# Kernel optimization log

Hardware: AMD Instinct MI355X
Metric: run time of the kernel (lower is better)

The kernel has to match this reference:

```python
import jax, jax.numpy as jnp
import numpy as np

# Sampled-block sizes (fanouts [25, 10], batch of 1024 seeds)
N_SRC1, N_DST1, N_E1 = 292864, 11264, 281600
N_DST2, N_E2 = 1024, 10240
IN, H, C = 256, 256, 47


def setup_inputs() -> dict:
    key = jax.random.key(0)
    ks = jax.random.split(key, 9)
    s_in = 1.0 / np.sqrt(IN)
    s_h = 1.0 / np.sqrt(H)
    x = jax.random.normal(ks[0], (N_SRC1, IN), jnp.float32)
    src1 = jax.random.randint(ks[1], (N_E1,), 0, N_SRC1)
    dst1 = jnp.sort(jax.random.randint(ks[2], (N_E1,), 0, N_DST1))
    src2 = jax.random.randint(ks[3], (N_E2,), 0, N_DST1)
    dst2 = jnp.sort(jax.random.randint(ks[4], (N_E2,), 0, N_DST2))
    return dict(
        x=x, src1=src1, dst1=dst1, src2=src2, dst2=dst2,
        W_self1=jax.random.normal(ks[5], (IN, H), jnp.float32) * s_in,
        W_neigh1=jax.random.normal(ks[6], (IN, H), jnp.float32) * s_in,
        b1=jnp.zeros((H,), jnp.float32),
        W_self2=jax.random.normal(ks[7], (H, C), jnp.float32) * s_h,
        W_neigh2=jax.random.normal(ks[8], (H, C), jnp.float32) * s_h,
        b2=jnp.zeros((C,), jnp.float32),
    )


def _sage_mean(h_src, src, dst, n_dst, W_self, W_neigh, b):
    # DGL SAGEConv(mean): out = fc_self(h_dst) + fc_neigh(mean_{neighbors} h_src) + b
    gathered = h_src[src]                                   # [E, F] gather
    agg = jax.ops.segment_sum(gathered, dst, num_segments=n_dst)
    deg = jax.ops.segment_sum(jnp.ones((src.shape[0],), h_src.dtype), dst,
                              num_segments=n_dst)
    h_neigh = agg / jnp.maximum(deg, 1.0)[:, None]          # mean aggregation
    h_dst = h_src[:n_dst]                                   # dst nodes are prefix of src
    return h_dst @ W_self + h_neigh @ W_neigh + b


def reference(x, src1, dst1, src2, dst2,
              W_self1, W_neigh1, b1, W_self2, W_neigh2, b2):
    h = _sage_mean(x, src1, dst1, N_DST1, W_self1, W_neigh1, b1)
    h = jax.nn.relu(h)  # dropout is identity in eval mode
    out = _sage_mean(h, src2, dst2, N_DST2, W_self2, W_neigh2, b2)
    return out
```

## Files before the change

### kernel.cpp

```cpp
#include <hip/hip_runtime.h>

#define NSRC1 292864
#define NDST1 11264
#define NE1   281600
#define NDST2 1024
#define NE2   10240

__global__ __launch_bounds__(64) void agg_kernel(
    const float* __restrict__ feat,
    const int*   __restrict__ src_idx,
    const int*   __restrict__ dst_idx,
    int n_edges,
    float* __restrict__ out)
{
    const int d = blockIdx.x;

    int lo = 0, hi = n_edges;
    while (lo < hi) { int mid = (lo + hi) >> 1; if (dst_idx[mid] <  d) lo = mid + 1; else hi = mid; }
    const int start = lo;
    hi = n_edges;
    while (lo < hi) { int mid = (lo + hi) >> 1; if (dst_idx[mid] <= d) lo = mid + 1; else hi = mid; }
    const int end = lo;

    const int c4 = threadIdx.x;
    float4 acc = make_float4(0.f, 0.f, 0.f, 0.f);
    for (int e = start; e < end; ++e) {
        const int s = src_idx[e];
        const float4 v = ((const float4*)(feat + (size_t)s * 256))[c4];
        acc.x += v.x; acc.y += v.y; acc.z += v.z; acc.w += v.w;
    }
    const int deg = end - start;
    const float inv = 1.0f / (deg > 0 ? (float)deg : 1.0f);
    acc.x *= inv; acc.y *= inv; acc.z *= inv; acc.w *= inv;
    ((float4*)(out + (size_t)d * 256))[c4] = acc;
}

__global__ __launch_bounds__(256) void gemm1_kernel(
    const float* __restrict__ x,
    const float* __restrict__ hn,
    const float* __restrict__ Ws,
    const float* __restrict__ Wn,
    const float* __restrict__ b,
    float* __restrict__ h)
{
    __shared__ float As[64][17];
    __shared__ float Bs[16][64];

    const int tid = threadIdx.x;
    const int tx = tid & 15, ty = tid >> 4;
    const int mblk = blockIdx.x * 64, nblk = blockIdx.y * 64;

    float acc[4][4] = {};

    const float* Aptr[2] = { x, hn };
    const float* Bptr[2] = { Ws, Wn };

    for (int phase = 0; phase < 2; ++phase) {
        const float* __restrict__ A = Aptr[phase];
        const float* __restrict__ B = Bptr[phase];
        for (int kt = 0; kt < 256; kt += 16) {
            {
                const int ar = tid >> 2, ak = (tid & 3) << 2;
                const float4 av = *(const float4*)(A + (size_t)(mblk + ar) * 256 + kt + ak);
                As[ar][ak + 0] = av.x; As[ar][ak + 1] = av.y;
                As[ar][ak + 2] = av.z; As[ar][ak + 3] = av.w;
            }
            {
                const int br = tid >> 4, bn = (tid & 15) << 2;
                const float4 bv = *(const float4*)(B + (size_t)(kt + br) * 256 + nblk + bn);
                *(float4*)&Bs[br][bn] = bv;
            }
            __syncthreads();
            #pragma unroll
            for (int kk = 0; kk < 16; ++kk) {
                float a0 = As[ty * 4 + 0][kk];
                float a1 = As[ty * 4 + 1][kk];
                float a2 = As[ty * 4 + 2][kk];
                float a3 = As[ty * 4 + 3][kk];
                float b0 = Bs[kk][tx * 4 + 0];
                float b1 = Bs[kk][tx * 4 + 1];
                float b2 = Bs[kk][tx * 4 + 2];
                float b3 = Bs[kk][tx * 4 + 3];
                acc[0][0] += a0 * b0; acc[0][1] += a0 * b1; acc[0][2] += a0 * b2; acc[0][3] += a0 * b3;
                acc[1][0] += a1 * b0; acc[1][1] += a1 * b1; acc[1][2] += a1 * b2; acc[1][3] += a1 * b3;
                acc[2][0] += a2 * b0; acc[2][1] += a2 * b1; acc[2][2] += a2 * b2; acc[2][3] += a2 * b3;
                acc[3][0] += a3 * b0; acc[3][1] += a3 * b1; acc[3][2] += a3 * b2; acc[3][3] += a3 * b3;
            }
            __syncthreads();
        }
    }

    #pragma unroll
    for (int i = 0; i < 4; ++i) {
        const int m = mblk + ty * 4 + i;
        #pragma unroll
        for (int j = 0; j < 4; ++j) {
            const int n = nblk + tx * 4 + j;
            float v = acc[i][j] + b[n];
            h[(size_t)m * 256 + n] = v > 0.f ? v : 0.f;
        }
    }
}

__global__ __launch_bounds__(64) void out_kernel(
    const float* __restrict__ h,
    const float* __restrict__ hn2,
    const float* __restrict__ Ws,
    const float* __restrict__ Wn,
    const float* __restrict__ b,
    float* __restrict__ out)
{
    const int m = blockIdx.x;
    const int c = threadIdx.x;
    if (c >= 47) return;
    float acc = b[c];
    const float* __restrict__ hrow  = h   + (size_t)m * 256;
    const float* __restrict__ hnrow = hn2 + (size_t)m * 256;
    for (int k = 0; k < 256; ++k) {
        acc += hrow[k] * Ws[k * 47 + c] + hnrow[k] * Wn[k * 47 + c];
    }
    out[(size_t)m * 47 + c] = acc;
}

extern "C" void kernel_launch(void* const* d_in, const int* in_sizes, int n_in,
                              void* d_out, int out_size, void* d_ws, size_t ws_size,
                              hipStream_t stream) {
    const float* x    = (const float*)d_in[0];
    const int*   src1 = (const int*)  d_in[1];
    const int*   dst1 = (const int*)  d_in[2];
    const int*   src2 = (const int*)  d_in[3];
    const int*   dst2 = (const int*)  d_in[4];
    const float* Ws1  = (const float*)d_in[5];
    const float* Wn1  = (const float*)d_in[6];
    const float* b1   = (const float*)d_in[7];
    const float* Ws2  = (const float*)d_in[8];
    const float* Wn2  = (const float*)d_in[9];
    const float* b2   = (const float*)d_in[10];
    float* out = (float*)d_out;

    char* ws = (char*)d_ws;
    const size_t sz_h1 = (size_t)NDST1 * 256 * sizeof(float);
    float* hn1 = (float*)(ws);
    float* h   = (float*)(ws + sz_h1);
    float* hn2 = (float*)(ws + 2 * sz_h1);

    agg_kernel<<<NDST1, 64, 0, stream>>>(x, src1, dst1, NE1, hn1);
    dim3 g1(NDST1 / 64, 256 / 64);
    gemm1_kernel<<<g1, 256, 0, stream>>>(x, hn1, Ws1, Wn1, b1, h);
    agg_kernel<<<NDST2, 64, 0, stream>>>(h, src2, dst2, NE2, hn2);
    out_kernel<<<NDST2, 64, 0, stream>>>(h, hn2, Ws2, Wn2, b2, out);
}
```

Before: 498.2 us.

## Use bf16 MFMA for layer-1 GEMM with fused aggregation and concatenated operand

```diff
diff --git a/kernel.cpp b/kernel.cpp
--- a/kernel.cpp
+++ b/kernel.cpp
@@ -6,19 +6,158 @@
 #define NDST2 1024
 #define NE2   10240
 
-__global__ __launch_bounds__(64) void agg_kernel(
+typedef __bf16 bf16x8 __attribute__((ext_vector_type(8)));
+typedef float  f32x4  __attribute__((ext_vector_type(4)));
+
+__device__ __forceinline__ unsigned short f2bf(float f) {
+    union { float f; unsigned u; } v; v.f = f;
+    unsigned r = v.u + 0x7FFF + ((v.u >> 16) & 1);
+    return (unsigned short)(r >> 16);
+}
+
+__global__ __launch_bounds__(256) void agg1_fused_kernel(
+    const float* __restrict__ x,
+    const int*   __restrict__ src_idx,
+    const int*   __restrict__ dst_idx,
+    unsigned short* __restrict__ Abf)
+{
+    const int lane = threadIdx.x & 63;
+    const int w    = threadIdx.x >> 6;
+    const int d    = blockIdx.x * 4 + w;
+
+    int lo = 0, hi = NE1;
+    while (lo < hi) { int mid = (lo + hi) >> 1; if (dst_idx[mid] <  d) lo = mid + 1; else hi = mid; }
+    const int start = lo;
+    hi = NE1;
+    while (lo < hi) { int mid = (lo + hi) >> 1; if (dst_idx[mid] <= d) lo = mid + 1; else hi = mid; }
+    const int end = lo;
+
+    float4 acc = make_float4(0.f, 0.f, 0.f, 0.f);
+    for (int e = start; e < end; ++e) {
+        const int s = src_idx[e];
+        const float4 v = ((const float4*)(x + (size_t)s * 256))[lane];
+        acc.x += v.x; acc.y += v.y; acc.z += v.z; acc.w += v.w;
+    }
+    const int deg = end - start;
+    const float inv = 1.0f / (deg > 0 ? (float)deg : 1.0f);
+
+    ushort4 nb;
+    nb.x = f2bf(acc.x * inv); nb.y = f2bf(acc.y * inv);
+    nb.z = f2bf(acc.z * inv); nb.w = f2bf(acc.w * inv);
+    *(ushort4*)(Abf + (size_t)d * 512 + 256 + lane * 4) = nb;
+
+    const float4 xv = ((const float4*)(x + (size_t)d * 256))[lane];
+    ushort4 sf;
+    sf.x = f2bf(xv.x); sf.y = f2bf(xv.y); sf.z = f2bf(xv.z); sf.w = f2bf(xv.w);
+    *(ushort4*)(Abf + (size_t)d * 512 + lane * 4) = sf;
+}
+
+__global__ __launch_bounds__(256) void prep_wt_kernel(
+    const float* __restrict__ Ws, const float* __restrict__ Wn,
+    unsigned short* __restrict__ Wt)
+{
+    __shared__ float t[64][65];
+    const int kb = blockIdx.x * 64, nb = blockIdx.y * 64;
+    const float* __restrict__ W = (kb < 256) ? Ws : Wn;
+    const int kofs = (kb < 256) ? kb : kb - 256;
+    const int c  = threadIdx.x & 63;
+    const int r0 = threadIdx.x >> 6;
+    #pragma unroll
+    for (int i = 0; i < 16; ++i) {
+        const int r = r0 + i * 4;
+        t[r][c] = W[(size_t)(kofs + r) * 256 + nb + c];
+    }
+    __syncthreads();
+    #pragma unroll
+    for (int i = 0; i < 16; ++i) {
+        const int r = r0 + i * 4;
+        Wt[(size_t)(nb + r) * 512 + kb + c] = f2bf(t[c][r]);
+    }
+}
+
+#define LDT 40
+
+__global__ __launch_bounds__(256) void gemm1_mfma_kernel(
+    const unsigned short* __restrict__ Abf,
+    const unsigned short* __restrict__ Wt,
+    const float* __restrict__ bias,
+    float* __restrict__ h)
+{
+    __shared__ unsigned short As[128][LDT];
+    __shared__ unsigned short Bs[64][LDT];
+
+    const int tid  = threadIdx.x;
+    const int lane = tid & 63;
+    const int w    = tid >> 6;
+    const int wm   = (w & 1) * 64;
+    const int wn   = (w >> 1) * 32;
+    const int mblk = blockIdx.x * 128;
+    const int nblk = blockIdx.y * 64;
+
+    const int r16 = lane & 15;
+    const int k0  = (lane >> 4) * 8;
+
+    f32x4 acc[4][2] = {};
+
+    for (int kt = 0; kt < 512; kt += 32) {
+        #pragma unroll
+        for (int i = 0; i < 2; ++i) {
+            const int idx = tid + i * 256;
+            const int r  = idx >> 2;
+            const int kk = (idx & 3) * 8;
+            *(uint4*)&As[r][kk] =
+                *(const uint4*)(Abf + (size_t)(mblk + r) * 512 + kt + kk);
+        }
+        {
+            const int r  = tid >> 2;
+            const int kk = (tid & 3) * 8;
+            *(uint4*)&Bs[r][kk] =
+                *(const uint4*)(Wt + (size_t)(nblk + r) * 512 + kt + kk);
+        }
+        __syncthreads();
+
+        bf16x8 bfrag[2];
+        #pragma unroll
+        for (int ni = 0; ni < 2; ++ni)
+            bfrag[ni] = *(const bf16x8*)&Bs[wn + ni * 16 + r16][k0];
+        #pragma unroll
+        for (int mi = 0; mi < 4; ++mi) {
+            const bf16x8 afrag = *(const bf16x8*)&As[wm + mi * 16 + r16][k0];
+            #pragma unroll
+            for (int ni = 0; ni < 2; ++ni)
+                acc[mi][ni] = __builtin_amdgcn_mfma_f32_16x16x32_bf16(
+                    afrag, bfrag[ni], acc[mi][ni], 0, 0, 0);
+        }
+        __syncthreads();
+    }
+
+    #pragma unroll
+    for (int mi = 0; mi < 4; ++mi) {
+        #pragma unroll
+        for (int ni = 0; ni < 2; ++ni) {
+            const int col = nblk + wn + ni * 16 + r16;
+            const float bb = bias[col];
+            #pragma unroll
+            for (int r = 0; r < 4; ++r) {
+                const int row = mblk + wm + mi * 16 + (lane >> 4) * 4 + r;
+                const float v = acc[mi][ni][r] + bb;
+                h[(size_t)row * 256 + col] = v > 0.f ? v : 0.f;
+            }
+        }
+    }
+}
+
+__global__ __launch_bounds__(64) void agg2_kernel(
     const float* __restrict__ feat,
     const int*   __restrict__ src_idx,
     const int*   __restrict__ dst_idx,
-    int n_edges,
     float* __restrict__ out)
 {
     const int d = blockIdx.x;
-
-    int lo = 0, hi = n_edges;
+    int lo = 0, hi = NE2;
     while (lo < hi) { int mid = (lo + hi) >> 1; if (dst_idx[mid] <  d) lo = mid + 1; else hi = mid; }
     const int start = lo;
-    hi = n_edges;
+    hi = NE2;
     while (lo < hi) { int mid = (lo + hi) >> 1; if (dst_idx[mid] <= d) lo = mid + 1; else hi = mid; }
     const int end = lo;
 
@@ -33,73 +172,6 @@
     const float inv = 1.0f / (deg > 0 ? (float)deg : 1.0f);
     acc.x *= inv; acc.y *= inv; acc.z *= inv; acc.w *= inv;
     ((float4*)(out + (size_t)d * 256))[c4] = acc;
-}
-
-__global__ __launch_bounds__(256) void gemm1_kernel(
-    const float* __restrict__ x,
-    const float* __restrict__ hn,
-    const float* __restrict__ Ws,
-    const float* __restrict__ Wn,
-    const float* __restrict__ b,
-    float* __restrict__ h)
-{
-    __shared__ float As[64][17];
-    __shared__ float Bs[16][64];
-
-    const int tid = threadIdx.x;
-    const int tx = tid & 15, ty = tid >> 4;
-    const int mblk = blockIdx.x * 64, nblk = blockIdx.y * 64;
-
-    float acc[4][4] = {};
-
-    const float* Aptr[2] = { x, hn };
-    const float* Bptr[2] = { Ws, Wn };
-
-    for (int phase = 0; phase < 2; ++phase) {
-        const float* __restrict__ A = Aptr[phase];
-        const float* __restrict__ B = Bptr[phase];
-        for (int kt = 0; kt < 256; kt += 16) {
-            {
-                const int ar = tid >> 2, ak = (tid & 3) << 2;
-                const float4 av = *(const float4*)(A + (size_t)(mblk + ar) * 256 + kt + ak);
-                As[ar][ak + 0] = av.x; As[ar][ak + 1] = av.y;
-                As[ar][ak + 2] = av.z; As[ar][ak + 3] = av.w;
-            }
-            {
-                const int br = tid >> 4, bn = (tid & 15) << 2;
-                const float4 bv = *(const float4*)(B + (size_t)(kt + br) * 256 + nblk + bn);
-                *(float4*)&Bs[br][bn] = bv;
-            }
-            __syncthreads();
-            #pragma unroll
-            for (int kk = 0; kk < 16; ++kk) {
-                float a0 = As[ty * 4 + 0][kk];
-                float a1 = As[ty * 4 + 1][kk];
-                float a2 = As[ty * 4 + 2][kk];
-                float a3 = As[ty * 4 + 3][kk];
-                float b0 = Bs[kk][tx * 4 + 0];
-                float b1 = Bs[kk][tx * 4 + 1];
-                float b2 = Bs[kk][tx * 4 + 2];
-                float b3 = Bs[kk][tx * 4 + 3];
-                acc[0][0] += a0 * b0; acc[0][1] += a0 * b1; acc[0][2] += a0 * b2; acc[0][3] += a0 * b3;
-                acc[1][0] += a1 * b0; acc[1][1] += a1 * b1; acc[1][2] += a1 * b2; acc[1][3] += a1 * b3;
-                acc[2][0] += a2 * b0; acc[2][1] += a2 * b1; acc[2][2] += a2 * b2; acc[2][3] += a2 * b3;
-                acc[3][0] += a3 * b0; acc[3][1] += a3 * b1; acc[3][2] += a3 * b2; acc[3][3] += a3 * b3;
-            }
-            __syncthreads();
-        }
-    }
-
-    #pragma unroll
-    for (int i = 0; i < 4; ++i) {
-        const int m = mblk + ty * 4 + i;
-        #pragma unroll
-        for (int j = 0; j < 4; ++j) {
-            const int n = nblk + tx * 4 + j;
-            float v = acc[i][j] + b[n];
-            h[(size_t)m * 256 + n] = v > 0.f ? v : 0.f;
-        }
-    }
 }
 
 __global__ __launch_bounds__(64) void out_kernel(
@@ -139,14 +211,19 @@
     float* out = (float*)d_out;
 
     char* ws = (char*)d_ws;
-    const size_t sz_h1 = (size_t)NDST1 * 256 * sizeof(float);
-    float* hn1 = (float*)(ws);
-    float* h   = (float*)(ws + sz_h1);
-    float* hn2 = (float*)(ws + 2 * sz_h1);
-
-    agg_kernel<<<NDST1, 64, 0, stream>>>(x, src1, dst1, NE1, hn1);
-    dim3 g1(NDST1 / 64, 256 / 64);
-    gemm1_kernel<<<g1, 256, 0, stream>>>(x, hn1, Ws1, Wn1, b1, h);
-    agg_kernel<<<NDST2, 64, 0, stream>>>(h, src2, dst2, NE2, hn2);
+    const size_t sz_Abf = (size_t)NDST1 * 512 * sizeof(unsigned short);
+    const size_t sz_h   = (size_t)NDST1 * 256 * sizeof(float);
+    const size_t sz_hn2 = (size_t)NDST2 * 256 * sizeof(float);
+    unsigned short* Abf = (unsigned short*)(ws);
+    float*          h   = (float*)(ws + sz_Abf);
+    float*          hn2 = (float*)(ws + sz_Abf + sz_h);
+    unsigned short* Wt  = (unsigned short*)(ws + sz_Abf + sz_h + sz_hn2);
+
+    dim3 gw(8, 4);
+    prep_wt_kernel<<<gw, 256, 0, stream>>>(Ws1, Wn1, Wt);
+    agg1_fused_kernel<<<NDST1 / 4, 256, 0, stream>>>(x, src1, dst1, Abf);
+    dim3 g1(NDST1 / 128, 256 / 64);
+    gemm1_mfma_kernel<<<g1, 256, 0, stream>>>(Abf, Wt, b1, h);
+    agg2_kernel<<<NDST2, 64, 0, stream>>>(h, src2, dst2, hn2);
     out_kernel<<<NDST2, 64, 0, stream>>>(h, hn2, Ws2, Wn2, b2, out);
 }
```

New measurement: 483.4 us. -3.0%, faster.
